# Kernel tuning notes

Measured on AMD Instinct MI355X. Metric: run time of the kernel, lower is better.

Reference implementation:

```python
import jax, jax.numpy as jnp
import numpy as np

N, E = 50000, 600000
D_IN, D_H, D_OUT = 512, 128, 1
BN_EPS = 1e-5


def setup_inputs() -> dict:
    key = jax.random.key(0)
    ks = jax.random.split(key, 16)
    s = 0.05
    inp = {
        "feature": jax.random.normal(ks[0], (N, D_IN), dtype=jnp.float32),
        "edge_index": jax.random.randint(ks[1], (2, E), 0, N, dtype=jnp.int32),
        "head_W": jax.random.normal(ks[2], (D_IN, D_H), dtype=jnp.float32) * s,
        "head_b": jnp.zeros((D_H,), dtype=jnp.float32),
        "gin_W1": jax.random.normal(ks[3], (D_H, D_H), dtype=jnp.float32) * s,
        "gin_b1": jnp.zeros((D_H,), dtype=jnp.float32),
        "lin_W1": jax.random.normal(ks[4], (D_H, D_H), dtype=jnp.float32) * s,
        "lin_b1": jnp.zeros((D_H,), dtype=jnp.float32),
        "gin_W2": jax.random.normal(ks[5], (D_H, D_H), dtype=jnp.float32) * s,
        "gin_b2": jnp.zeros((D_H,), dtype=jnp.float32),
        "lin_W2": jax.random.normal(ks[6], (D_H, D_H), dtype=jnp.float32) * s,
        "lin_b2": jnp.zeros((D_H,), dtype=jnp.float32),
        "tail_W": jax.random.normal(ks[7], (D_H, D_OUT), dtype=jnp.float32) * s,
        "tail_b": jnp.zeros((D_OUT,), dtype=jnp.float32),
        "bn_gamma": jnp.ones((D_OUT,), dtype=jnp.float32),
        "bn_beta": jnp.zeros((D_OUT,), dtype=jnp.float32),
    }
    return inp


def _gin_layer(x, src, dst, gin_W, gin_b, lin_W, lin_b):
    # PyG GINConv, eps=0: nn((1+eps)*x + sum_{j in N(i)} x_j)
    agg = jax.ops.segment_sum(x[src], dst, num_segments=N)  # [N, D_H]
    h = jax.nn.relu((x + agg) @ gin_W + gin_b)              # GIN MLP (dropout p=0)
    return h @ lin_W + lin_b                                # plain post-linear


def reference(feature, edge_index, head_W, head_b,
              gin_W1, gin_b1, lin_W1, lin_b1,
              gin_W2, gin_b2, lin_W2, lin_b2,
              tail_W, tail_b, bn_gamma, bn_beta):
    src, dst = edge_index[0], edge_index[1]
    x = jax.nn.relu(feature @ head_W + head_b)              # head block (dropout p=0)
    x = _gin_layer(x, src, dst, gin_W1, gin_b1, lin_W1, lin_b1)
    x = _gin_layer(x, src, dst, gin_W2, gin_b2, lin_W2, lin_b2)
    z = x @ tail_W + tail_b                                 # [N, 1]
    # BatchNorm1d in training mode: biased batch stats over the node dim
    mu = jnp.mean(z, axis=0, keepdims=True)
    var = jnp.mean((z - mu) ** 2, axis=0, keepdims=True)
    return (z - mu) * jax.lax.rsqrt(var + BN_EPS) * bn_gamma + bn_beta
```

## Files before the change

### kernel.cpp

```cpp
#include <hip/hip_runtime.h>

#define N_NODES 50000
#define N_EDGES 600000
#define DH 128
#define BN_EPS 1e-5f
#define SCAN_BLOCKS ((N_NODES + 255) / 256)

typedef __attribute__((ext_vector_type(8))) short bf16x8;
typedef __attribute__((ext_vector_type(4))) float f32x4;

__device__ inline unsigned short f2bf(float x) {
  unsigned u = __float_as_uint(x);
  return (unsigned short)((u + 0x7FFFu + ((u >> 16) & 1u)) >> 16);
}
__device__ inline float bf2f(unsigned short h) {
  return __uint_as_float(((unsigned)h) << 16);
}

__device__ inline void gl_lds16(const unsigned short* g, unsigned short* l) {
  __builtin_amdgcn_global_load_lds(
      (const __attribute__((address_space(1))) unsigned int*)g,
      (__attribute__((address_space(3))) unsigned int*)l, 16, 0, 0);
}

__global__ __launch_bounds__(256) void convert_W5(
    const float* __restrict__ hW, const float* __restrict__ g1,
    const float* __restrict__ l1, const float* __restrict__ g2,
    const float* __restrict__ l2,
    unsigned short* __restrict__ hH, unsigned short* __restrict__ hL,
    unsigned short* __restrict__ g1H, unsigned short* __restrict__ g1L,
    unsigned short* __restrict__ l1H, unsigned short* __restrict__ l1L,
    unsigned short* __restrict__ g2H, unsigned short* __restrict__ g2L,
    unsigned short* __restrict__ l2H, unsigned short* __restrict__ l2L) {
  int b = blockIdx.x;
  const float* W;
  unsigned short *hi, *lo;
  int idx;
  if (b < 256) {
    W = hW; hi = hH; lo = hL;
    idx = b * 256 + threadIdx.x;
  } else {
    int w = (b - 256) >> 6;
    idx = ((b - 256) & 63) * 256 + threadIdx.x;
    W = (w == 0) ? g1 : (w == 1) ? l1 : (w == 2) ? g2 : l2;
    hi = (w == 0) ? g1H : (w == 1) ? l1H : (w == 2) ? g2H : l2H;
    lo = (w == 0) ? g1L : (w == 1) ? l1L : (w == 2) ? g2L : l2L;
  }
  int k = idx >> 7;
  int n = idx & 127;
  float x = W[idx];
  unsigned short h = f2bf(x);
  unsigned short l = f2bf(x - bf2f(h));
  int kstep = k >> 5;
  int ctile = ((n >> 6) << 2) | (n & 3);
  int cs = (n >> 2) & 15;
  int lane = ((k >> 3) & 3) * 16 + cs;
  int j = k & 7;
  size_t off = ((size_t)(kstep * 8 + ctile) * 64 + lane) * 8 + j;
  hi[off] = h;
  lo[off] = l;
}

__global__ __launch_bounds__(256) void gemm_head(const float* __restrict__ A,
                                                 const unsigned short* __restrict__ Bh,
                                                 const unsigned short* __restrict__ Bl,
                                                 const float* __restrict__ bias,
                                                 float* __restrict__ C,
                                                 unsigned short* __restrict__ xb_out,
                                                 int M) {
  constexpr int K = 512;
  constexpr int KSTEPS = K / 64;
  constexpr int ASTR = 72;
  __shared__ __align__(16) unsigned short Ah[64 * ASTR];
  __shared__ __align__(16) unsigned short Bhs[2][4096];
  __shared__ __align__(16) unsigned short Bls[2][4096];

  const int tid = threadIdx.x;
  const int wave = tid >> 6;
  const int lane = tid & 63;
  const int m0 = blockIdx.x * 64;

  const int s_row = tid >> 2;
  const int s_grp = tid & 3;
  const int g_row = m0 + s_row;
  const int g_rowc = (g_row < M) ? g_row : (M - 1);
  const float* af = A + (size_t)g_rowc * K + s_grp * 16;

  const int rgrp = wave & 1;
  const int ch = wave >> 1;

  f32x4 acc[2][4];
#pragma unroll
  for (int r = 0; r < 2; ++r)
#pragma unroll
    for (int c = 0; c < 4; ++c) acc[r][c] = (f32x4){0.f, 0.f, 0.f, 0.f};

  for (int ks = 0; ks < KSTEPS; ++ks) {
    {
      float4 f0 = *(const float4*)(af + ks * 64);
      float4 f1 = *(const float4*)(af + ks * 64 + 4);
      float4 f2 = *(const float4*)(af + ks * 64 + 8);
      float4 f3 = *(const float4*)(af + ks * 64 + 12);
      ushort4 h0, h1, h2, h3;
      h0.x = f2bf(f0.x); h0.y = f2bf(f0.y); h0.z = f2bf(f0.z); h0.w = f2bf(f0.w);
      h1.x = f2bf(f1.x); h1.y = f2bf(f1.y); h1.z = f2bf(f1.z); h1.w = f2bf(f1.w);
      h2.x = f2bf(f2.x); h2.y = f2bf(f2.y); h2.z = f2bf(f2.z); h2.w = f2bf(f2.w);
      h3.x = f2bf(f3.x); h3.y = f2bf(f3.y); h3.z = f2bf(f3.z); h3.w = f2bf(f3.w);
      int base = s_row * ASTR + s_grp * 16;
      *(ushort4*)&Ah[base + 0] = h0;
      *(ushort4*)&Ah[base + 4] = h1;
      *(ushort4*)&Ah[base + 8] = h2;
      *(ushort4*)&Ah[base + 12] = h3;
    }
#pragma unroll
    for (int s = 0; s < 2; ++s) {
      const unsigned short* sh = Bh + (size_t)(2 * ks + s) * 4096 + wave * 1024;
      const unsigned short* sl = Bl + (size_t)(2 * ks + s) * 4096 + wave * 1024;
      gl_lds16(sh + lane * 8, &Bhs[s][wave * 1024]);
      gl_lds16(sh + 512 + lane * 8, &Bhs[s][wave * 1024 + 512]);
      gl_lds16(sl + lane * 8, &Bls[s][wave * 1024]);
      gl_lds16(sl + 512 + lane * 8, &Bls[s][wave * 1024 + 512]);
    }
    __syncthreads();

#pragma unroll
    for (int s = 0; s < 2; ++s) {
      bf16x8 a0 = *(const bf16x8*)&Ah[(rgrp * 32 + (lane & 15)) * ASTR + s * 32 + (lane >> 4) * 8];
      bf16x8 a1 = *(const bf16x8*)&Ah[(rgrp * 32 + 16 + (lane & 15)) * ASTR + s * 32 + (lane >> 4) * 8];
#pragma unroll
      for (int c = 0; c < 4; ++c) {
        int ct = ch * 4 + c;
        bf16x8 bh = *(const bf16x8*)&Bhs[s][(ct * 64 + lane) * 8];
        bf16x8 bl = *(const bf16x8*)&Bls[s][(ct * 64 + lane) * 8];
        acc[0][c] = __builtin_amdgcn_mfma_f32_16x16x32_bf16(a0, bh, acc[0][c], 0, 0, 0);
        acc[0][c] = __builtin_amdgcn_mfma_f32_16x16x32_bf16(a0, bl, acc[0][c], 0, 0, 0);
        acc[1][c] = __builtin_amdgcn_mfma_f32_16x16x32_bf16(a1, bh, acc[1][c], 0, 0, 0);
        acc[1][c] = __builtin_amdgcn_mfma_f32_16x16x32_bf16(a1, bl, acc[1][c], 0, 0, 0);
      }
    }
    __syncthreads();
  }

  const int coln = lane & 15;
  const int rown = (lane >> 4) * 4;
  const int colbase = ch * 64 + coln * 4;
  const float4 bv = *(const float4*)(bias + colbase);
#pragma unroll
  for (int r = 0; r < 2; ++r) {
#pragma unroll
    for (int reg = 0; reg < 4; ++reg) {
      int row = m0 + rgrp * 32 + r * 16 + rown + reg;
      if (row < M) {
        float4 v;
        v.x = fmaxf(acc[r][0][reg] + bv.x, 0.f);
        v.y = fmaxf(acc[r][1][reg] + bv.y, 0.f);
        v.z = fmaxf(acc[r][2][reg] + bv.z, 0.f);
        v.w = fmaxf(acc[r][3][reg] + bv.w, 0.f);
        *(float4*)&C[(size_t)row * DH + colbase] = v;
        ushort4 hb;
        hb.x = f2bf(v.x); hb.y = f2bf(v.y); hb.z = f2bf(v.z); hb.w = f2bf(v.w);
        *(ushort4*)&xb_out[(size_t)row * DH + colbase] = hb;
      }
    }
  }
}

__global__ __launch_bounds__(256) void gemm_gin(
    const unsigned short* __restrict__ yb,
    const unsigned short* __restrict__ B1h, const unsigned short* __restrict__ B1l,
    const float* __restrict__ b1,
    const unsigned short* __restrict__ B2h, const unsigned short* __restrict__ B2l,
    const float* __restrict__ b2, float* __restrict__ X,
    unsigned short* __restrict__ xb_out, int M) {
  constexpr int K = 128;
  constexpr int KSTEPS = K / 32;
  constexpr int ASTR = 40;
  constexpr int HSTR = 136;
  __shared__ __align__(16) unsigned short Ah[64 * ASTR];
  __shared__ __align__(16) unsigned short Bhs[4096];
  __shared__ __align__(16) unsigned short Bls[4096];
  __shared__ __align__(16) unsigned short Hb[64 * HSTR];

  const int tid = threadIdx.x;
  const int wave = tid >> 6;
  const int lane = tid & 63;
  const int m0 = blockIdx.x * 64;

  const int s_row = tid >> 2;
  const int s_oct = tid & 3;
  const int g_row = m0 + s_row;
  const int g_rowc = (g_row < M) ? g_row : (M - 1);
  const unsigned short* ab = yb + (size_t)g_rowc * K + s_oct * 8;

  const int rgrp = wave & 1;
  const int ch = wave >> 1;
  const int coln = lane & 15;
  const int rown = (lane >> 4) * 4;
  const int colbase = ch * 64 + coln * 4;

  auto issueB = [&](const unsigned short* Bh, const unsigned short* Bl, int ks) {
    const unsigned short* sh = Bh + (size_t)ks * 4096 + wave * 1024;
    const unsigned short* sl = Bl + (size_t)ks * 4096 + wave * 1024;
    gl_lds16(sh + lane * 8, &Bhs[wave * 1024]);
    gl_lds16(sh + 512 + lane * 8, &Bhs[wave * 1024 + 512]);
    gl_lds16(sl + lane * 8, &Bls[wave * 1024]);
    gl_lds16(sl + 512 + lane * 8, &Bls[wave * 1024 + 512]);
  };

  f32x4 acc[2][4];
#pragma unroll
  for (int r = 0; r < 2; ++r)
#pragma unroll
    for (int c = 0; c < 4; ++c) acc[r][c] = (f32x4){0.f, 0.f, 0.f, 0.f};

  for (int ks = 0; ks < KSTEPS; ++ks) {
    *(uint4*)&Ah[s_row * ASTR + s_oct * 8] = *(const uint4*)(ab + ks * 32);
    issueB(B1h, B1l, ks);
    __syncthreads();
    bf16x8 a0 = *(const bf16x8*)&Ah[(rgrp * 32 + (lane & 15)) * ASTR + (lane >> 4) * 8];
    bf16x8 a1 = *(const bf16x8*)&Ah[(rgrp * 32 + 16 + (lane & 15)) * ASTR + (lane >> 4) * 8];
#pragma unroll
    for (int c = 0; c < 4; ++c) {
      int ct = ch * 4 + c;
      bf16x8 bh = *(const bf16x8*)&Bhs[(ct * 64 + lane) * 8];
      bf16x8 bl = *(const bf16x8*)&Bls[(ct * 64 + lane) * 8];
      acc[0][c] = __builtin_amdgcn_mfma_f32_16x16x32_bf16(a0, bh, acc[0][c], 0, 0, 0);
      acc[0][c] = __builtin_amdgcn_mfma_f32_16x16x32_bf16(a0, bl, acc[0][c], 0, 0, 0);
      acc[1][c] = __builtin_amdgcn_mfma_f32_16x16x32_bf16(a1, bh, acc[1][c], 0, 0, 0);
      acc[1][c] = __builtin_amdgcn_mfma_f32_16x16x32_bf16(a1, bl, acc[1][c], 0, 0, 0);
    }
    __syncthreads();
  }

  {
    const float4 bv = *(const float4*)(b1 + colbase);
#pragma unroll
    for (int r = 0; r < 2; ++r) {
#pragma unroll
      for (int reg = 0; reg < 4; ++reg) {
        int lrow = rgrp * 32 + r * 16 + rown + reg;
        ushort4 hb;
        hb.x = f2bf(fmaxf(acc[r][0][reg] + bv.x, 0.f));
        hb.y = f2bf(fmaxf(acc[r][1][reg] + bv.y, 0.f));
        hb.z = f2bf(fmaxf(acc[r][2][reg] + bv.z, 0.f));
        hb.w = f2bf(fmaxf(acc[r][3][reg] + bv.w, 0.f));
        *(ushort4*)&Hb[lrow * HSTR + colbase] = hb;
      }
    }
#pragma unroll
    for (int r = 0; r < 2; ++r)
#pragma unroll
      for (int c = 0; c < 4; ++c) acc[r][c] = (f32x4){0.f, 0.f, 0.f, 0.f};
  }

  for (int ks = 0; ks < KSTEPS; ++ks) {
    issueB(B2h, B2l, ks);
    __syncthreads();
    bf16x8 a0 = *(const bf16x8*)&Hb[(rgrp * 32 + (lane & 15)) * HSTR + ks * 32 + (lane >> 4) * 8];
    bf16x8 a1 = *(const bf16x8*)&Hb[(rgrp * 32 + 16 + (lane & 15)) * HSTR + ks * 32 + (lane >> 4) * 8];
#pragma unroll
    for (int c = 0; c < 4; ++c) {
      int ct = ch * 4 + c;
      bf16x8 bh = *(const bf16x8*)&Bhs[(ct * 64 + lane) * 8];
      bf16x8 bl = *(const bf16x8*)&Bls[(ct * 64 + lane) * 8];
      acc[0][c] = __builtin_amdgcn_mfma_f32_16x16x32_bf16(a0, bh, acc[0][c], 0, 0, 0);
      acc[0][c] = __builtin_amdgcn_mfma_f32_16x16x32_bf16(a0, bl, acc[0][c], 0, 0, 0);
      acc[1][c] = __builtin_amdgcn_mfma_f32_16x16x32_bf16(a1, bh, acc[1][c], 0, 0, 0);
      acc[1][c] = __builtin_amdgcn_mfma_f32_16x16x32_bf16(a1, bl, acc[1][c], 0, 0, 0);
    }
    __syncthreads();
  }

  {
    const float4 bv = *(const float4*)(b2 + colbase);
#pragma unroll
    for (int r = 0; r < 2; ++r) {
#pragma unroll
      for (int reg = 0; reg < 4; ++reg) {
        int row = m0 + rgrp * 32 + r * 16 + rown + reg;
        if (row < M) {
          float4 v;
          v.x = acc[r][0][reg] + bv.x;
          v.y = acc[r][1][reg] + bv.y;
          v.z = acc[r][2][reg] + bv.z;
          v.w = acc[r][3][reg] + bv.w;
          *(float4*)&X[(size_t)row * DH + colbase] = v;
          if (xb_out) {
            ushort4 hb;
            hb.x = f2bf(v.x); hb.y = f2bf(v.y); hb.z = f2bf(v.z); hb.w = f2bf(v.w);
            *(ushort4*)&xb_out[(size_t)row * DH + colbase] = hb;
          }
        }
      }
    }
  }
}

__global__ __launch_bounds__(256) void count_deg(const int* __restrict__ eidx,
                                                 int* __restrict__ cnt) {
  int e = blockIdx.x * 256 + threadIdx.x;
  if (e < N_EDGES) atomicAdd(&cnt[eidx[N_EDGES + e]], 1);
}

__global__ __launch_bounds__(256) void scan_block(const int* __restrict__ cnt,
                                                  int* __restrict__ rs,
                                                  int* __restrict__ partials) {
  int t = threadIdx.x;
  int i = blockIdx.x * 256 + t;
  int v = (i < N_NODES) ? cnt[i] : 0;
  __shared__ int s[256];
  s[t] = v;
  __syncthreads();
#pragma unroll
  for (int off = 1; off < 256; off <<= 1) {
    int add = (t >= off) ? s[t - off] : 0;
    __syncthreads();
    s[t] += add;
    __syncthreads();
  }
  if (i < N_NODES) rs[i] = s[t] - v;
  if (t == 255) partials[blockIdx.x] = s[255];
}

__global__ __launch_bounds__(256) void scan_partials(int* __restrict__ partials) {
  int t = threadIdx.x;
  int v = (t < SCAN_BLOCKS) ? partials[t] : 0;
  __shared__ int s[256];
  s[t] = v;
  __syncthreads();
#pragma unroll
  for (int off = 1; off < 256; off <<= 1) {
    int add = (t >= off) ? s[t - off] : 0;
    __syncthreads();
    s[t] += add;
    __syncthreads();
  }
  if (t < SCAN_BLOCKS) partials[t] = s[t] - v;
}

__global__ __launch_bounds__(256) void add_offsets(int* __restrict__ rs,
                                                   const int* __restrict__ partials) {
  int i = blockIdx.x * 256 + threadIdx.x;
  if (i < N_NODES) rs[i] += partials[blockIdx.x];
  if (i == 0) rs[N_NODES] = N_EDGES;
}

__global__ __launch_bounds__(256) void fill_csr(const int* __restrict__ eidx,
                                                const int* __restrict__ rs,
                                                int* __restrict__ cursor,
                                                int* __restrict__ esrc) {
  int e = blockIdx.x * 256 + threadIdx.x;
  if (e >= N_EDGES) return;
  int d = eidx[N_EDGES + e];
  int p = atomicAdd(&cursor[d], 1);
  esrc[rs[d] + p] = eidx[e];
}

__global__ __launch_bounds__(256) void gin_aggregate_bf16(
    const unsigned short* __restrict__ xb, const float* __restrict__ x,
    const int* __restrict__ rs, const int* __restrict__ esrc,
    unsigned* __restrict__ yb) {
  int node = blockIdx.x * 4 + (threadIdx.x >> 6);
  int lane = threadIdx.x & 63;
  if (node >= N_NODES) return;
  float2 acc = ((const float2*)x)[(size_t)node * 64 + lane];
  const unsigned* xb2 = (const unsigned*)xb;
  int beg = rs[node];
  int end = rs[node + 1];
  int j = beg;
  for (; j + 8 <= end; j += 8) {
    int s0 = esrc[j + 0];
    int s1 = esrc[j + 1];
    int s2 = esrc[j + 2];
    int s3 = esrc[j + 3];
    int s4 = esrc[j + 4];
    int s5 = esrc[j + 5];
    int s6 = esrc[j + 6];
    int s7 = esrc[j + 7];
    unsigned v0 = xb2[(size_t)s0 * 64 + lane];
    unsigned v1 = xb2[(size_t)s1 * 64 + lane];
    unsigned v2 = xb2[(size_t)s2 * 64 + lane];
    unsigned v3 = xb2[(size_t)s3 * 64 + lane];
    unsigned v4 = xb2[(size_t)s4 * 64 + lane];
    unsigned v5 = xb2[(size_t)s5 * 64 + lane];
    unsigned v6 = xb2[(size_t)s6 * 64 + lane];
    unsigned v7 = xb2[(size_t)s7 * 64 + lane];
    acc.x += ((__uint_as_float(v0 << 16) + __uint_as_float(v1 << 16)) +
              (__uint_as_float(v2 << 16) + __uint_as_float(v3 << 16))) +
             ((__uint_as_float(v4 << 16) + __uint_as_float(v5 << 16)) +
              (__uint_as_float(v6 << 16) + __uint_as_float(v7 << 16)));
    acc.y += ((__uint_as_float(v0 & 0xFFFF0000u) + __uint_as_float(v1 & 0xFFFF0000u)) +
              (__uint_as_float(v2 & 0xFFFF0000u) + __uint_as_float(v3 & 0xFFFF0000u))) +
             ((__uint_as_float(v4 & 0xFFFF0000u) + __uint_as_float(v5 & 0xFFFF0000u)) +
              (__uint_as_float(v6 & 0xFFFF0000u) + __uint_as_float(v7 & 0xFFFF0000u)));
  }
  for (; j + 4 <= end; j += 4) {
    int s0 = esrc[j + 0];
    int s1 = esrc[j + 1];
    int s2 = esrc[j + 2];
    int s3 = esrc[j + 3];
    unsigned v0 = xb2[(size_t)s0 * 64 + lane];
    unsigned v1 = xb2[(size_t)s1 * 64 + lane];
    unsigned v2 = xb2[(size_t)s2 * 64 + lane];
    unsigned v3 = xb2[(size_t)s3 * 64 + lane];
    acc.x += (__uint_as_float(v0 << 16) + __uint_as_float(v1 << 16)) +
             (__uint_as_float(v2 << 16) + __uint_as_float(v3 << 16));
    acc.y += (__uint_as_float(v0 & 0xFFFF0000u) + __uint_as_float(v1 & 0xFFFF0000u)) +
             (__uint_as_float(v2 & 0xFFFF0000u) + __uint_as_float(v3 & 0xFFFF0000u));
  }
  for (; j < end; ++j) {
    unsigned v = xb2[(size_t)esrc[j] * 64 + lane];
    acc.x += __uint_as_float(v << 16);
    acc.y += __uint_as_float(v & 0xFFFF0000u);
  }
  yb[(size_t)node * 64 + lane] =
      (unsigned)f2bf(acc.x) | ((unsigned)f2bf(acc.y) << 16);
}

__global__ __launch_bounds__(256) void tail_bn1(const float* __restrict__ x,
                                                const float* __restrict__ tw,
                                                const float* __restrict__ tb,
                                                float* __restrict__ z,
                                                float* __restrict__ red) {
  const int lane = threadIdx.x & 31;
  const int grp = threadIdx.x >> 5;
  float4 w = *(const float4*)(tw + lane * 4);
  float accS = 0.f, accQ = 0.f;
  for (int node = blockIdx.x * 8 + grp; node < N_NODES; node += gridDim.x * 8) {
    float4 v = *(const float4*)(x + (size_t)node * DH + lane * 4);
    float p = v.x * w.x + v.y * w.y + v.z * w.z + v.w * w.w;
#pragma unroll
    for (int m = 16; m; m >>= 1) p += __shfl_xor(p, m, 32);
    if (lane == 0) {
      float zv = p + tb[0];
      z[node] = zv;
      accS += zv;
      accQ += zv * zv;
    }
  }
  __shared__ float sS[256];
  __shared__ float sQ[256];
  sS[threadIdx.x] = accS;
  sQ[threadIdx.x] = accQ;
  __syncthreads();
  for (int s = 128; s; s >>= 1) {
    if (threadIdx.x < s) {
      sS[threadIdx.x] += sS[threadIdx.x + s];
      sQ[threadIdx.x] += sQ[threadIdx.x + s];
    }
    __syncthreads();
  }
  if (threadIdx.x == 0) {
    atomicAdd(&red[0], sS[0]);
    atomicAdd(&red[1], sQ[0]);
  }
}

__global__ __launch_bounds__(256) void bn2(const float* __restrict__ z,
                                           const float* __restrict__ red,
                                           const float* __restrict__ gamma,
                                           const float* __restrict__ beta,
                                           float* __restrict__ out) {
  int i = blockIdx.x * 256 + threadIdx.x;
  if (i >= N_NODES) return;
  float mu = red[0] * (1.0f / N_NODES);
  float var = red[1] * (1.0f / N_NODES) - mu * mu;
  out[i] = (z[i] - mu) * rsqrtf(var + BN_EPS) * gamma[0] + beta[0];
}

extern "C" void kernel_launch(void* const* d_in, const int* in_sizes, int n_in,
                              void* d_out, int out_size, void* d_ws, size_t ws_size,
                              hipStream_t stream) {
  const float* feature = (const float*)d_in[0];
  const int* eidx = (const int*)d_in[1];
  const float* head_W = (const float*)d_in[2];
  const float* head_b = (const float*)d_in[3];
  const float* gin_W1 = (const float*)d_in[4];
  const float* gin_b1 = (const float*)d_in[5];
  const float* lin_W1 = (const float*)d_in[6];
  const float* lin_b1 = (const float*)d_in[7];
  const float* gin_W2 = (const float*)d_in[8];
  const float* gin_b2 = (const float*)d_in[9];
  const float* lin_W2 = (const float*)d_in[10];
  const float* lin_b2 = (const float*)d_in[11];
  const float* tail_W = (const float*)d_in[12];
  const float* tail_b = (const float*)d_in[13];
  const float* bn_gamma = (const float*)d_in[14];
  const float* bn_beta = (const float*)d_in[15];

  float* X = (float*)d_ws;
  float* z = X + (size_t)N_NODES * DH;
  float* red = z + N_NODES;
  int* row_start = (int*)(red + 2);
  int* cnt = row_start + (N_NODES + 1);
  int* partials = cnt + N_NODES;
  int* esrc = partials + 256;
  unsigned short* wp =
      (unsigned short*)(((uintptr_t)(esrc + N_EDGES) + 15) & ~(uintptr_t)15);
  unsigned short* hH = wp;
  unsigned short* hL = hH + 65536;
  unsigned short* g1H = hL + 65536;
  unsigned short* g1L = g1H + 16384;
  unsigned short* l1H = g1L + 16384;
  unsigned short* l1L = l1H + 16384;
  unsigned short* g2H = l1L + 16384;
  unsigned short* g2L = g2H + 16384;
  unsigned short* l2H = g2L + 16384;
  unsigned short* l2L = l2H + 16384;
  unsigned short* xb = l2L + 16384;
  unsigned short* yb = xb + (size_t)N_NODES * DH;

  const int gemm_grid = (N_NODES + 63) / 64;
  const int edge_grid = (N_EDGES + 255) / 256;
  const int agg_grid = (N_NODES + 3) / 4;

  convert_W5<<<512, 256, 0, stream>>>(head_W, gin_W1, lin_W1, gin_W2, lin_W2,
                                      hH, hL, g1H, g1L, l1H, l1L, g2H, g2L,
                                      l2H, l2L);

  hipMemsetAsync(cnt, 0, N_NODES * sizeof(int), stream);
  hipMemsetAsync(red, 0, 2 * sizeof(float), stream);
  count_deg<<<edge_grid, 256, 0, stream>>>(eidx, cnt);
  scan_block<<<SCAN_BLOCKS, 256, 0, stream>>>(cnt, row_start, partials);
  scan_partials<<<1, 256, 0, stream>>>(partials);
  add_offsets<<<SCAN_BLOCKS, 256, 0, stream>>>(row_start, partials);
  hipMemsetAsync(cnt, 0, N_NODES * sizeof(int), stream);
  fill_csr<<<edge_grid, 256, 0, stream>>>(eidx, row_start, cnt, esrc);

  gemm_head<<<gemm_grid, 256, 0, stream>>>(feature, hH, hL, head_b, X, xb,
                                           N_NODES);

  gin_aggregate_bf16<<<agg_grid, 256, 0, stream>>>(xb, X, row_start, esrc,
                                                   (unsigned*)yb);
  gemm_gin<<<gemm_grid, 256, 0, stream>>>(yb, g1H, g1L, gin_b1, l1H, l1L,
                                          lin_b1, X, xb, N_NODES);

  gin_aggregate_bf16<<<agg_grid, 256, 0, stream>>>(xb, X, row_start, esrc,
                                                   (unsigned*)yb);
  gemm_gin<<<gemm_grid, 256, 0, stream>>>(yb, g2H, g2L, gin_b2, l2H, l2L,
                                          lin_b2, X, nullptr, N_NODES);

  tail_bn1<<<256, 256, 0, stream>>>(X, tail_W, tail_b, z, red);
  bn2<<<(N_NODES + 255) / 256, 256, 0, stream>>>(z, red, bn_gamma, bn_beta, (float*)d_out);
}
```

Baseline: 399.0 us.

## Fuse degree counting into weight conversion; shrink head GEMM K-step to 32

The degree-count atomics now run as extra blocks of the weight-conversion kernel, which removes one kernel launch. The head GEMM goes from a 64-wide K tile with two B sub-stages to a single 32-wide K tile. That cuts shared memory use, which may allow more resident blocks, but it doubles the number of K iterations and __syncthreads barriers. Each iteration also has fewer loads in flight, so latency hiding could get worse.

```diff
diff --git a/kernel.cpp b/kernel.cpp
--- a/kernel.cpp
+++ b/kernel.cpp
@@ -23,7 +23,7 @@
       (__attribute__((address_space(3))) unsigned int*)l, 16, 0, 0);
 }
 
-__global__ __launch_bounds__(256) void convert_W5(
+__global__ __launch_bounds__(256) void convert_W5_count(
     const float* __restrict__ hW, const float* __restrict__ g1,
     const float* __restrict__ l1, const float* __restrict__ g2,
     const float* __restrict__ l2,
@@ -31,8 +31,14 @@
     unsigned short* __restrict__ g1H, unsigned short* __restrict__ g1L,
     unsigned short* __restrict__ l1H, unsigned short* __restrict__ l1L,
     unsigned short* __restrict__ g2H, unsigned short* __restrict__ g2L,
-    unsigned short* __restrict__ l2H, unsigned short* __restrict__ l2L) {
+    unsigned short* __restrict__ l2H, unsigned short* __restrict__ l2L,
+    const int* __restrict__ eidx, int* __restrict__ cnt) {
   int b = blockIdx.x;
+  if (b >= 512) {
+    int e = (b - 512) * 256 + threadIdx.x;
+    if (e < N_EDGES) atomicAdd(&cnt[eidx[N_EDGES + e]], 1);
+    return;
+  }
   const float* W;
   unsigned short *hi, *lo;
   int idx;
@@ -69,11 +75,11 @@
                                                  unsigned short* __restrict__ xb_out,
                                                  int M) {
   constexpr int K = 512;
-  constexpr int KSTEPS = K / 64;
-  constexpr int ASTR = 72;
+  constexpr int KSTEPS = K / 32;
+  constexpr int ASTR = 40;
   __shared__ __align__(16) unsigned short Ah[64 * ASTR];
-  __shared__ __align__(16) unsigned short Bhs[2][4096];
-  __shared__ __align__(16) unsigned short Bls[2][4096];
+  __shared__ __align__(16) unsigned short Bhs[4096];
+  __shared__ __align__(16) unsigned short Bls[4096];
 
   const int tid = threadIdx.x;
   const int wave = tid >> 6;
@@ -84,7 +90,7 @@
   const int s_grp = tid & 3;
   const int g_row = m0 + s_row;
   const int g_rowc = (g_row < M) ? g_row : (M - 1);
-  const float* af = A + (size_t)g_rowc * K + s_grp * 16;
+  const float* af = A + (size_t)g_rowc * K + s_grp * 8;
 
   const int rgrp = wave & 1;
   const int ch = wave >> 1;
@@ -97,46 +103,36 @@
 
   for (int ks = 0; ks < KSTEPS; ++ks) {
     {
-      float4 f0 = *(const float4*)(af + ks * 64);
-      float4 f1 = *(const float4*)(af + ks * 64 + 4);
-      float4 f2 = *(const float4*)(af + ks * 64 + 8);
-      float4 f3 = *(const float4*)(af + ks * 64 + 12);
-      ushort4 h0, h1, h2, h3;
+      float4 f0 = *(const float4*)(af + ks * 32);
+      float4 f1 = *(const float4*)(af + ks * 32 + 4);
+      ushort4 h0, h1;
       h0.x = f2bf(f0.x); h0.y = f2bf(f0.y); h0.z = f2bf(f0.z); h0.w = f2bf(f0.w);
       h1.x = f2bf(f1.x); h1.y = f2bf(f1.y); h1.z = f2bf(f1.z); h1.w = f2bf(f1.w);
-      h2.x = f2bf(f2.x); h2.y = f2bf(f2.y); h2.z = f2bf(f2.z); h2.w = f2bf(f2.w);
-      h3.x = f2bf(f3.x); h3.y = f2bf(f3.y); h3.z = f2bf(f3.z); h3.w = f2bf(f3.w);
-      int base = s_row * ASTR + s_grp * 16;
+      int base = s_row * ASTR + s_grp * 8;
       *(ushort4*)&Ah[base + 0] = h0;
       *(ushort4*)&Ah[base + 4] = h1;
-      *(ushort4*)&Ah[base + 8] = h2;
-      *(ushort4*)&Ah[base + 12] = h3;
-    }
-#pragma unroll
-    for (int s = 0; s < 2; ++s) {
-      const unsigned short* sh = Bh + (size_t)(2 * ks + s) * 4096 + wave * 1024;
-      const unsigned short* sl = Bl + (size_t)(2 * ks + s) * 4096 + wave * 1024;
-      gl_lds16(sh + lane * 8, &Bhs[s][wave * 1024]);
-      gl_lds16(sh + 512 + lane * 8, &Bhs[s][wave * 1024 + 512]);
-      gl_lds16(sl + lane * 8, &Bls[s][wave * 1024]);
-      gl_lds16(sl + 512 + lane * 8, &Bls[s][wave * 1024 + 512]);
-    }
-    __syncthreads();
-
-#pragma unroll
-    for (int s = 0; s < 2; ++s) {
-      bf16x8 a0 = *(const bf16x8*)&Ah[(rgrp * 32 + (lane & 15)) * ASTR + s * 32 + (lane >> 4) * 8];
-      bf16x8 a1 = *(const bf16x8*)&Ah[(rgrp * 32 + 16 + (lane & 15)) * ASTR + s * 32 + (lane >> 4) * 8];
-#pragma unroll
-      for (int c = 0; c < 4; ++c) {
-        int ct = ch * 4 + c;
-        bf16x8 bh = *(const bf16x8*)&Bhs[s][(ct * 64 + lane) * 8];
-        bf16x8 bl = *(const bf16x8*)&Bls[s][(ct * 64 + lane) * 8];
-        acc[0][c] = __builtin_amdgcn_mfma_f32_16x16x32_bf16(a0, bh, acc[0][c], 0, 0, 0);
-        acc[0][c] = __builtin_amdgcn_mfma_f32_16x16x32_bf16(a0, bl, acc[0][c], 0, 0, 0);
-        acc[1][c] = __builtin_amdgcn_mfma_f32_16x16x32_bf16(a1, bh, acc[1][c], 0, 0, 0);
-        acc[1][c] = __builtin_amdgcn_mfma_f32_16x16x32_bf16(a1, bl, acc[1][c], 0, 0, 0);
-      }
+    }
+    {
+      const unsigned short* sh = Bh + (size_t)ks * 4096 + wave * 1024;
+      const unsigned short* sl = Bl + (size_t)ks * 4096 + wave * 1024;
+      gl_lds16(sh + lane * 8, &Bhs[wave * 1024]);
+      gl_lds16(sh + 512 + lane * 8, &Bhs[wave * 1024 + 512]);
+      gl_lds16(sl + lane * 8, &Bls[wave * 1024]);
+      gl_lds16(sl + 512 + lane * 8, &Bls[wave * 1024 + 512]);
+    }
+    __syncthreads();
+
+    bf16x8 a0 = *(const bf16x8*)&Ah[(rgrp * 32 + (lane & 15)) * ASTR + (lane >> 4) * 8];
+    bf16x8 a1 = *(const bf16x8*)&Ah[(rgrp * 32 + 16 + (lane & 15)) * ASTR + (lane >> 4) * 8];
+#pragma unroll
+    for (int c = 0; c < 4; ++c) {
+      int ct = ch * 4 + c;
+      bf16x8 bh = *(const bf16x8*)&Bhs[(ct * 64 + lane) * 8];
+      bf16x8 bl = *(const bf16x8*)&Bls[(ct * 64 + lane) * 8];
+      acc[0][c] = __builtin_amdgcn_mfma_f32_16x16x32_bf16(a0, bh, acc[0][c], 0, 0, 0);
+      acc[0][c] = __builtin_amdgcn_mfma_f32_16x16x32_bf16(a0, bl, acc[0][c], 0, 0, 0);
+      acc[1][c] = __builtin_amdgcn_mfma_f32_16x16x32_bf16(a1, bh, acc[1][c], 0, 0, 0);
+      acc[1][c] = __builtin_amdgcn_mfma_f32_16x16x32_bf16(a1, bl, acc[1][c], 0, 0, 0);
     }
     __syncthreads();
   }
@@ -294,12 +290,6 @@
       }
     }
   }
-}
-
-__global__ __launch_bounds__(256) void count_deg(const int* __restrict__ eidx,
-                                                 int* __restrict__ cnt) {
-  int e = blockIdx.x * 256 + threadIdx.x;
-  if (e < N_EDGES) atomicAdd(&cnt[eidx[N_EDGES + e]], 1);
 }
 
 __global__ __launch_bounds__(256) void scan_block(const int* __restrict__ cnt,
@@ -510,24 +500,25 @@
   unsigned short* xb = l2L + 16384;
   unsigned short* yb = xb + (size_t)N_NODES * DH;
 
+  const int head_grid = (N_NODES + 63) / 64;
   const int gemm_grid = (N_NODES + 63) / 64;
   const int edge_grid = (N_EDGES + 255) / 256;
   const int agg_grid = (N_NODES + 3) / 4;
 
-  convert_W5<<<512, 256, 0, stream>>>(head_W, gin_W1, lin_W1, gin_W2, lin_W2,
-                                      hH, hL, g1H, g1L, l1H, l1L, g2H, g2L,
-                                      l2H, l2L);
-
   hipMemsetAsync(cnt, 0, N_NODES * sizeof(int), stream);
   hipMemsetAsync(red, 0, 2 * sizeof(float), stream);
-  count_deg<<<edge_grid, 256, 0, stream>>>(eidx, cnt);
+
+  convert_W5_count<<<512 + edge_grid, 256, 0, stream>>>(
+      head_W, gin_W1, lin_W1, gin_W2, lin_W2, hH, hL, g1H, g1L, l1H, l1L,
+      g2H, g2L, l2H, l2L, eidx, cnt);
+
   scan_block<<<SCAN_BLOCKS, 256, 0, stream>>>(cnt, row_start, partials);
   scan_partials<<<1, 256, 0, stream>>>(partials);
   add_offsets<<<SCAN_BLOCKS, 256, 0, stream>>>(row_start, partials);
   hipMemsetAsync(cnt, 0, N_NODES * sizeof(int), stream);
   fill_csr<<<edge_grid, 256, 0, stream>>>(eidx, row_start, cnt, esrc);
 
-  gemm_head<<<gemm_grid, 256, 0, stream>>>(feature, hH, hL, head_b, X, xb,
+  gemm_head<<<head_grid, 256, 0, stream>>>(feature, hH, hL, head_b, X, xb,
                                            N_NODES);
 
   gin_aggregate_bf16<<<agg_grid, 256, 0, stream>>>(xb, X, row_start, esrc,
```

Measured after the change: 400.9 us. Within noise of the previous version (+0.5%).

## Fuse CSR build into weight-convert and head GEMM, pad neighbor lists to four

Applied to the files above, without the earlier changes.

Folds degree counting into the weight-conversion kernel and the CSR fill into extra blocks of the head GEMM, which cuts launches and memsets. Each node's neighbor list is padded to a multiple of four with a dummy node whose zeroed bf16 row sits past the real rows, so the aggregation can use int4 index loads and drop its scalar tail loop. The reduction buffer is now zeroed inside scan_partials and the tail kernel grid is doubled. The cost is about 25% more edge-slot gathers, which all hit the zero row, plus a new pad_fill kernel and tighter coupling between kernels.

```diff
diff --git a/kernel.cpp b/kernel.cpp
--- a/kernel.cpp
+++ b/kernel.cpp
@@ -5,6 +5,7 @@
 #define DH 128
 #define BN_EPS 1e-5f
 #define SCAN_BLOCKS ((N_NODES + 255) / 256)
+#define HEAD_GRID ((N_NODES + 63) / 64)
 
 typedef __attribute__((ext_vector_type(8))) short bf16x8;
 typedef __attribute__((ext_vector_type(4))) float f32x4;
@@ -23,7 +24,7 @@
       (__attribute__((address_space(3))) unsigned int*)l, 16, 0, 0);
 }
 
-__global__ __launch_bounds__(256) void convert_W5(
+__global__ __launch_bounds__(256) void convert_W5_count(
     const float* __restrict__ hW, const float* __restrict__ g1,
     const float* __restrict__ l1, const float* __restrict__ g2,
     const float* __restrict__ l2,
@@ -31,8 +32,14 @@
     unsigned short* __restrict__ g1H, unsigned short* __restrict__ g1L,
     unsigned short* __restrict__ l1H, unsigned short* __restrict__ l1L,
     unsigned short* __restrict__ g2H, unsigned short* __restrict__ g2L,
-    unsigned short* __restrict__ l2H, unsigned short* __restrict__ l2L) {
+    unsigned short* __restrict__ l2H, unsigned short* __restrict__ l2L,
+    const int* __restrict__ eidx, int* __restrict__ cnt) {
   int b = blockIdx.x;
+  if (b >= 512) {
+    int e = (b - 512) * 256 + threadIdx.x;
+    if (e < N_EDGES) atomicAdd(&cnt[eidx[N_EDGES + e]], 1);
+    return;
+  }
   const float* W;
   unsigned short *hi, *lo;
   int idx;
@@ -61,19 +68,29 @@
   lo[off] = l;
 }
 
-__global__ __launch_bounds__(256) void gemm_head(const float* __restrict__ A,
-                                                 const unsigned short* __restrict__ Bh,
-                                                 const unsigned short* __restrict__ Bl,
-                                                 const float* __restrict__ bias,
-                                                 float* __restrict__ C,
-                                                 unsigned short* __restrict__ xb_out,
-                                                 int M) {
+__global__ __launch_bounds__(256) void gemm_head_fill(
+    const float* __restrict__ A,
+    const unsigned short* __restrict__ Bh, const unsigned short* __restrict__ Bl,
+    const float* __restrict__ bias, float* __restrict__ C,
+    unsigned short* __restrict__ xb_out, int M,
+    const int* __restrict__ eidx, const int* __restrict__ rs,
+    int* __restrict__ cursor, int* __restrict__ esrc) {
   constexpr int K = 512;
   constexpr int KSTEPS = K / 64;
   constexpr int ASTR = 72;
   __shared__ __align__(16) unsigned short Ah[64 * ASTR];
   __shared__ __align__(16) unsigned short Bhs[2][4096];
   __shared__ __align__(16) unsigned short Bls[2][4096];
+
+  if (blockIdx.x >= HEAD_GRID) {
+    int e = (blockIdx.x - HEAD_GRID) * 256 + threadIdx.x;
+    if (e < N_EDGES) {
+      int d = eidx[N_EDGES + e];
+      int p = atomicAdd(&cursor[d], 1);
+      esrc[rs[d] + p] = eidx[e];
+    }
+    return;
+  }
 
   const int tid = threadIdx.x;
   const int wave = tid >> 6;
@@ -296,18 +313,12 @@
   }
 }
 
-__global__ __launch_bounds__(256) void count_deg(const int* __restrict__ eidx,
-                                                 int* __restrict__ cnt) {
-  int e = blockIdx.x * 256 + threadIdx.x;
-  if (e < N_EDGES) atomicAdd(&cnt[eidx[N_EDGES + e]], 1);
-}
-
 __global__ __launch_bounds__(256) void scan_block(const int* __restrict__ cnt,
                                                   int* __restrict__ rs,
                                                   int* __restrict__ partials) {
   int t = threadIdx.x;
   int i = blockIdx.x * 256 + t;
-  int v = (i < N_NODES) ? cnt[i] : 0;
+  int v = (i < N_NODES) ? ((cnt[i] + 3) & ~3) : 0;
   __shared__ int s[256];
   s[t] = v;
   __syncthreads();
@@ -322,8 +333,10 @@
   if (t == 255) partials[blockIdx.x] = s[255];
 }
 
-__global__ __launch_bounds__(256) void scan_partials(int* __restrict__ partials) {
+__global__ __launch_bounds__(256) void scan_partials(int* __restrict__ partials,
+                                                     float* __restrict__ red) {
   int t = threadIdx.x;
+  if (t == 0) { red[0] = 0.f; red[1] = 0.f; }
   int v = (t < SCAN_BLOCKS) ? partials[t] : 0;
   __shared__ int s[256];
   s[t] = v;
@@ -339,21 +352,26 @@
 }
 
 __global__ __launch_bounds__(256) void add_offsets(int* __restrict__ rs,
-                                                   const int* __restrict__ partials) {
+                                                   const int* __restrict__ partials,
+                                                   const int* __restrict__ cnt) {
   int i = blockIdx.x * 256 + threadIdx.x;
-  if (i < N_NODES) rs[i] += partials[blockIdx.x];
-  if (i == 0) rs[N_NODES] = N_EDGES;
-}
-
-__global__ __launch_bounds__(256) void fill_csr(const int* __restrict__ eidx,
-                                                const int* __restrict__ rs,
-                                                int* __restrict__ cursor,
+  if (i < N_NODES) {
+    int v = rs[i] + partials[blockIdx.x];
+    rs[i] = v;
+    if (i == N_NODES - 1) rs[N_NODES] = v + ((cnt[i] + 3) & ~3);
+  }
+}
+
+__global__ __launch_bounds__(256) void pad_fill(const int* __restrict__ rs,
+                                                int* __restrict__ cnt,
                                                 int* __restrict__ esrc) {
-  int e = blockIdx.x * 256 + threadIdx.x;
-  if (e >= N_EDGES) return;
-  int d = eidx[N_EDGES + e];
-  int p = atomicAdd(&cursor[d], 1);
-  esrc[rs[d] + p] = eidx[e];
+  int i = blockIdx.x * 256 + threadIdx.x;
+  if (i >= N_NODES) return;
+  int d = cnt[i];
+  cnt[i] = 0;
+  int b = rs[i] + d;
+  int e = rs[i + 1];
+  for (int k = b; k < e; ++k) esrc[k] = N_NODES;
 }
 
 __global__ __launch_bounds__(256) void gin_aggregate_bf16(
@@ -369,22 +387,16 @@
   int end = rs[node + 1];
   int j = beg;
   for (; j + 8 <= end; j += 8) {
-    int s0 = esrc[j + 0];
-    int s1 = esrc[j + 1];
-    int s2 = esrc[j + 2];
-    int s3 = esrc[j + 3];
-    int s4 = esrc[j + 4];
-    int s5 = esrc[j + 5];
-    int s6 = esrc[j + 6];
-    int s7 = esrc[j + 7];
-    unsigned v0 = xb2[(size_t)s0 * 64 + lane];
-    unsigned v1 = xb2[(size_t)s1 * 64 + lane];
-    unsigned v2 = xb2[(size_t)s2 * 64 + lane];
-    unsigned v3 = xb2[(size_t)s3 * 64 + lane];
-    unsigned v4 = xb2[(size_t)s4 * 64 + lane];
-    unsigned v5 = xb2[(size_t)s5 * 64 + lane];
-    unsigned v6 = xb2[(size_t)s6 * 64 + lane];
-    unsigned v7 = xb2[(size_t)s7 * 64 + lane];
+    int4 ia = *(const int4*)&esrc[j];
+    int4 ib = *(const int4*)&esrc[j + 4];
+    unsigned v0 = xb2[(size_t)ia.x * 64 + lane];
+    unsigned v1 = xb2[(size_t)ia.y * 64 + lane];
+    unsigned v2 = xb2[(size_t)ia.z * 64 + lane];
+    unsigned v3 = xb2[(size_t)ia.w * 64 + lane];
+    unsigned v4 = xb2[(size_t)ib.x * 64 + lane];
+    unsigned v5 = xb2[(size_t)ib.y * 64 + lane];
+    unsigned v6 = xb2[(size_t)ib.z * 64 + lane];
+    unsigned v7 = xb2[(size_t)ib.w * 64 + lane];
     acc.x += ((__uint_as_float(v0 << 16) + __uint_as_float(v1 << 16)) +
               (__uint_as_float(v2 << 16) + __uint_as_float(v3 << 16))) +
              ((__uint_as_float(v4 << 16) + __uint_as_float(v5 << 16)) +
@@ -394,24 +406,16 @@
              ((__uint_as_float(v4 & 0xFFFF0000u) + __uint_as_float(v5 & 0xFFFF0000u)) +
               (__uint_as_float(v6 & 0xFFFF0000u) + __uint_as_float(v7 & 0xFFFF0000u)));
   }
-  for (; j + 4 <= end; j += 4) {
-    int s0 = esrc[j + 0];
-    int s1 = esrc[j + 1];
-    int s2 = esrc[j + 2];
-    int s3 = esrc[j + 3];
-    unsigned v0 = xb2[(size_t)s0 * 64 + lane];
-    unsigned v1 = xb2[(size_t)s1 * 64 + lane];
-    unsigned v2 = xb2[(size_t)s2 * 64 + lane];
-    unsigned v3 = xb2[(size_t)s3 * 64 + lane];
+  if (j < end) {
+    int4 ia = *(const int4*)&esrc[j];
+    unsigned v0 = xb2[(size_t)ia.x * 64 + lane];
+    unsigned v1 = xb2[(size_t)ia.y * 64 + lane];
+    unsigned v2 = xb2[(size_t)ia.z * 64 + lane];
+    unsigned v3 = xb2[(size_t)ia.w * 64 + lane];
     acc.x += (__uint_as_float(v0 << 16) + __uint_as_float(v1 << 16)) +
              (__uint_as_float(v2 << 16) + __uint_as_float(v3 << 16));
     acc.y += (__uint_as_float(v0 & 0xFFFF0000u) + __uint_as_float(v1 & 0xFFFF0000u)) +
              (__uint_as_float(v2 & 0xFFFF0000u) + __uint_as_float(v3 & 0xFFFF0000u));
-  }
-  for (; j < end; ++j) {
-    unsigned v = xb2[(size_t)esrc[j] * 64 + lane];
-    acc.x += __uint_as_float(v << 16);
-    acc.y += __uint_as_float(v & 0xFFFF0000u);
   }
   yb[(size_t)node * 64 + lane] =
       (unsigned)f2bf(acc.x) | ((unsigned)f2bf(acc.y) << 16);
@@ -494,9 +498,9 @@
   int* row_start = (int*)(red + 2);
   int* cnt = row_start + (N_NODES + 1);
   int* partials = cnt + N_NODES;
-  int* esrc = partials + 256;
+  int* esrc = (int*)(((uintptr_t)(partials + 256) + 15) & ~(uintptr_t)15);
   unsigned short* wp =
-      (unsigned short*)(((uintptr_t)(esrc + N_EDGES) + 15) & ~(uintptr_t)15);
+      (unsigned short*)(((uintptr_t)(esrc + 760000) + 15) & ~(uintptr_t)15);
   unsigned short* hH = wp;
   unsigned short* hL = hH + 65536;
   unsigned short* g1H = hL + 65536;
@@ -508,38 +512,37 @@
   unsigned short* l2H = g2L + 16384;
   unsigned short* l2L = l2H + 16384;
   unsigned short* xb = l2L + 16384;
-  unsigned short* yb = xb + (size_t)N_NODES * DH;
-
-  const int gemm_grid = (N_NODES + 63) / 64;
+  unsigned short* yb = xb + (size_t)(N_NODES + 1) * DH;
+
+  const int gin_grid = (N_NODES + 63) / 64;
   const int edge_grid = (N_EDGES + 255) / 256;
   const int agg_grid = (N_NODES + 3) / 4;
 
-  convert_W5<<<512, 256, 0, stream>>>(head_W, gin_W1, lin_W1, gin_W2, lin_W2,
-                                      hH, hL, g1H, g1L, l1H, l1L, g2H, g2L,
-                                      l2H, l2L);
-
   hipMemsetAsync(cnt, 0, N_NODES * sizeof(int), stream);
-  hipMemsetAsync(red, 0, 2 * sizeof(float), stream);
-  count_deg<<<edge_grid, 256, 0, stream>>>(eidx, cnt);
+  hipMemsetAsync(xb + (size_t)N_NODES * DH, 0, DH * sizeof(unsigned short), stream);
+
+  convert_W5_count<<<512 + edge_grid, 256, 0, stream>>>(
+      head_W, gin_W1, lin_W1, gin_W2, lin_W2, hH, hL, g1H, g1L, l1H, l1L,
+      g2H, g2L, l2H, l2L, eidx, cnt);
+
   scan_block<<<SCAN_BLOCKS, 256, 0, stream>>>(cnt, row_start, partials);
-  scan_partials<<<1, 256, 0, stream>>>(partials);
-  add_offsets<<<SCAN_BLOCKS, 256, 0, stream>>>(row_start, partials);
-  hipMemsetAsync(cnt, 0, N_NODES * sizeof(int), stream);
-  fill_csr<<<edge_grid, 256, 0, stream>>>(eidx, row_start, cnt, esrc);
-
-  gemm_head<<<gemm_grid, 256, 0, stream>>>(feature, hH, hL, head_b, X, xb,
-                                           N_NODES);
+  scan_partials<<<1, 256, 0, stream>>>(partials, red);
+  add_offsets<<<SCAN_BLOCKS, 256, 0, stream>>>(row_start, partials, cnt);
+  pad_fill<<<SCAN_BLOCKS, 256, 0, stream>>>(row_start, cnt, esrc);
+
+  gemm_head_fill<<<HEAD_GRID + edge_grid, 256, 0, stream>>>(
+      feature, hH, hL, head_b, X, xb, N_NODES, eidx, row_start, cnt, esrc);
 
   gin_aggregate_bf16<<<agg_grid, 256, 0, stream>>>(xb, X, row_start, esrc,
                                                    (unsigned*)yb);
-  gemm_gin<<<gemm_grid, 256, 0, stream>>>(yb, g1H, g1L, gin_b1, l1H, l1L,
-                                          lin_b1, X, xb, N_NODES);
+  gemm_gin<<<gin_grid, 256, 0, stream>>>(yb, g1H, g1L, gin_b1, l1H, l1L,
+                                         lin_b1, X, xb, N_NODES);
 
   gin_aggregate_bf16<<<agg_grid, 256, 0, stream>>>(xb, X, row_start, esrc,
                                                    (unsigned*)yb);
-  gemm_gin<<<gemm_grid, 256, 0, stream>>>(yb, g2H, g2L, gin_b2, l2H, l2L,
-                                          lin_b2, X, nullptr, N_NODES);
-
-  tail_bn1<<<256, 256, 0, stream>>>(X, tail_W, tail_b, z, red);
+  gemm_gin<<<gin_grid, 256, 0, stream>>>(yb, g2H, g2L, gin_b2, l2H, l2L,
+                                         lin_b2, X, nullptr, N_NODES);
+
+  tail_bn1<<<512, 256, 0, stream>>>(X, tail_W, tail_b, z, red);
   bn2<<<(N_NODES + 255) / 256, 256, 0, stream>>>(z, red, bn_gamma, bn_beta, (float*)d_out);
 }
```

New measurement: 372.6 us. 1.07x faster.
